# Kernel tuning notes

Measured on AMD Instinct MI355X. Metric: run time of the kernel, lower is better.

## Reference

```python
import jax, jax.numpy as jnp
import numpy as np

N = 4096   # node_each_graph == in_feats (adjacency-row node features)
H = 512    # n_hidden
C = 2      # n_classes
E = 65536  # edges (avg degree 16)
NL = 5     # n_layers -> 4 GINConv layers
NR = NL - 2  # stacked hidden GIN layers (layers 1..3)


def _bn(x, g, b, m, v):
    # BatchNorm1d in eval mode (running stats), eps=1e-5
    return (x - m) * jax.lax.rsqrt(v + 1e-5) * g + b


def setup_inputs():
    key = jax.random.key(0)
    ks = iter(jax.random.split(key, 16))
    nk = lambda: next(ks)
    s = 0.02
    f32 = jnp.float32
    d = {}
    d["feat"] = jax.random.normal(nk(), (N, N), f32)
    d["edge_src"] = jax.random.randint(nk(), (E,), 0, N)
    d["edge_dst"] = jax.random.randint(nk(), (E,), 0, N)
    # GIN layer 0: MLP is Linear(N,H)-BN-ReLU-Linear(H,H); ApplyNodeFunc BN; outer BN
    d["eps0"] = jnp.zeros((), f32)
    d["W0a"] = jax.random.normal(nk(), (N, H), f32) * s
    d["b0a"] = jnp.zeros((H,), f32)
    d["W0b"] = jax.random.normal(nk(), (H, H), f32) * s
    d["b0b"] = jnp.zeros((H,), f32)
    for nm in ["bn0a", "bnA0", "bnO0"]:
        d[nm + "_g"] = jnp.ones((H,), f32); d[nm + "_b"] = jnp.zeros((H,), f32)
        d[nm + "_m"] = jnp.zeros((H,), f32); d[nm + "_v"] = jnp.ones((H,), f32)
    # GIN layers 1..NL-2 stacked (H -> H)
    d["epsR"] = jnp.zeros((NR,), f32)
    d["WRa"] = jax.random.normal(nk(), (NR, H, H), f32) * s
    d["bRa"] = jnp.zeros((NR, H), f32)
    d["WRb"] = jax.random.normal(nk(), (NR, H, H), f32) * s
    d["bRb"] = jnp.zeros((NR, H), f32)
    for nm in ["bnRa", "bnAR", "bnOR"]:
        d[nm + "_g"] = jnp.ones((NR, H), f32); d[nm + "_b"] = jnp.zeros((NR, H), f32)
        d[nm + "_m"] = jnp.zeros((NR, H), f32); d[nm + "_v"] = jnp.ones((NR, H), f32)
    # per-hidden-rep readout linears (batch_size = 1)
    d["Wp0"] = jax.random.normal(nk(), (N * N, C), f32) * 0.001
    d["bp0"] = jnp.zeros((C,), f32)
    d["WpR"] = jax.random.normal(nk(), (NL - 1, N * H, C), f32) * 0.001
    d["bpR"] = jnp.zeros((NL - 1, C), f32)
    return d


def _gin(h, src, dst, eps, Wa, ba, bna, Wb, bb, bnA, bnO):
    # GINConv sum-aggregation: (1+eps)*h + sum over in-neighbors
    agg = jax.ops.segment_sum(h[src], dst, num_segments=N)
    x = (1.0 + eps) * h + agg
    # MLP (num_layers=2): Linear -> BN -> ReLU -> Linear
    x = jax.nn.relu(_bn(x @ Wa + ba, *bna))
    x = x @ Wb + bb
    # ApplyNodeFunc: BN -> ReLU
    x = jax.nn.relu(_bn(x, *bnA))
    # Model-level BN -> ReLU
    x = jax.nn.relu(_bn(x, *bnO))
    return x


def reference(feat, edge_src, edge_dst, eps0, W0a, b0a, W0b, b0b,
              bn0a_g, bn0a_b, bn0a_m, bn0a_v, bnA0_g, bnA0_b, bnA0_m, bnA0_v,
              bnO0_g, bnO0_b, bnO0_m, bnO0_v,
              epsR, WRa, bRa, WRb, bRb,
              bnRa_g, bnRa_b, bnRa_m, bnRa_v, bnAR_g, bnAR_b, bnAR_m, bnAR_v,
              bnOR_g, bnOR_b, bnOR_m, bnOR_v, Wp0, bp0, WpR, bpR):
    h = _gin(feat, edge_src, edge_dst, eps0, W0a, b0a,
             (bn0a_g, bn0a_b, bn0a_m, bn0a_v), W0b, b0b,
             (bnA0_g, bnA0_b, bnA0_m, bnA0_v), (bnO0_g, bnO0_b, bnO0_m, bnO0_v))
    hs = [h]
    for i in range(NR):  # small fixed layer loop
        h = _gin(h, edge_src, edge_dst, epsR[i], WRa[i], bRa[i],
                 (bnRa_g[i], bnRa_b[i], bnRa_m[i], bnRa_v[i]), WRb[i], bRb[i],
                 (bnAR_g[i], bnAR_b[i], bnAR_m[i], bnAR_v[i]),
                 (bnOR_g[i], bnOR_b[i], bnOR_m[i], bnOR_v[i]))
        hs.append(h)
    # jumping-knowledge readout over hidden_rep (eval: dropout = identity)
    score = feat.reshape(1, -1) @ Wp0 + bp0
    for i, hi in enumerate(hs):
        score = score + hi.reshape(1, -1) @ WpR[i] + bpR[i]
    return score
```

## Files before the change

kernel.cpp:

```cpp
#include <hip/hip_runtime.h>
#include <cstdint>
#include <cstddef>

typedef __attribute__((ext_vector_type(8))) short short8;
typedef __attribute__((ext_vector_type(4))) float f32x4;
typedef __attribute__((ext_vector_type(4))) float f4;
typedef __attribute__((ext_vector_type(2))) float f2;
typedef __attribute__((ext_vector_type(4))) unsigned short us4;

#define NN 4096
#define HH 512
#define EE 65536

#define GLOAD(gp, lp) __builtin_amdgcn_global_load_lds( \
    (const __attribute__((address_space(1))) void*)(gp), \
    (__attribute__((address_space(3))) void*)(lp), 16, 0, 0)

__device__ __forceinline__ unsigned short f2bf(float x) {
    union { float f; unsigned u; } un; un.f = x;
    unsigned r = un.u + 0x7fffu + ((un.u >> 16) & 1u);
    return (unsigned short)(r >> 16);
}
__device__ __forceinline__ float b2f(unsigned short v) {
    union { unsigned u; float f; } un; un.u = ((unsigned)v) << 16; return un.f;
}

__global__ __launch_bounds__(256) void k_prep(const float* __restrict__ feat,
                                              const float* __restrict__ Wp0,
                                              unsigned short* __restrict__ featb,
                                              float* __restrict__ part,
                                              const float* __restrict__ W0a,
                                              const float* __restrict__ W0b,
                                              const float* __restrict__ WRa,
                                              const float* __restrict__ WRb,
                                              unsigned short* __restrict__ w0at,
                                              unsigned short* __restrict__ wt,
                                              const int* __restrict__ edst,
                                              int* __restrict__ starts,
                                              int* __restrict__ cursor) {
    __shared__ alignas(16) f4 fs[1024];
    __shared__ float s0[256], s1[256];
    __shared__ int wtot4[4], woff4[4];
    const int t = threadIdx.x;
    const int bid = blockIdx.x;
    if (bid == 0) {
        int* cnt = (int*)fs;
        for (int i = t; i < NN; i += 256) { cnt[i] = 0; cursor[i] = 0; }
        __syncthreads();
        const int4* e4 = (const int4*)edst;
        for (int b = 0; b < 64; b += 8) {
            int4 v[8];
#pragma unroll
            for (int k = 0; k < 8; ++k)
                v[k] = e4[(b + k) * 256 + t];
#pragma unroll
            for (int k = 0; k < 8; ++k) {
                atomicAdd(&cnt[v[k].x], 1); atomicAdd(&cnt[v[k].y], 1);
                atomicAdd(&cnt[v[k].z], 1); atomicAdd(&cnt[v[k].w], 1);
            }
        }
        __syncthreads();
        const int base = t * 16;
        int c[16]; int s = 0;
#pragma unroll
        for (int i = 0; i < 16; ++i) { c[i] = cnt[base + i]; s += c[i]; }
        const int lane = t & 63, wv = t >> 6;
        int inc = s;
        for (int d = 1; d < 64; d <<= 1) {
            int v = __shfl_up(inc, d);
            if (lane >= d) inc += v;
        }
        if (lane == 63) wtot4[wv] = inc;
        __syncthreads();
        if (t == 0) {
            int a = 0;
            for (int i = 0; i < 4; ++i) { woff4[i] = a; a += wtot4[i]; }
            starts[NN] = a;
        }
        __syncthreads();
        int run = woff4[wv] + inc - s;
#pragma unroll
        for (int i = 0; i < 16; ++i) { starts[base + i] = run; run += c[i]; }
    } else if (bid <= 4096) {
        const int b2 = bid - 1;
        const long B0 = (long)b2 * 1024;
        const f4* ff = (const f4*)feat;
        const f4* ww = (const f4*)Wp0;
        f4 v[4];
#pragma unroll
        for (int k = 0; k < 4; ++k)
            v[k] = __builtin_nontemporal_load(ff + B0 + k * 256 + t);
#pragma unroll
        for (int k = 0; k < 4; ++k) {
            fs[k * 256 + t] = v[k];
            us4 o;
            o.x = f2bf(v[k].x); o.y = f2bf(v[k].y); o.z = f2bf(v[k].z); o.w = f2bf(v[k].w);
            __builtin_nontemporal_store(o, (us4*)featb + B0 + k * 256 + t);
        }
        f4 wv[8];
#pragma unroll
        for (int k = 0; k < 8; ++k)
            wv[k] = __builtin_nontemporal_load(ww + 2 * B0 + k * 256 + t);
        __syncthreads();
        float a0 = 0.f, a1 = 0.f;
#pragma unroll
        for (int k = 0; k < 8; ++k) {
            const int q = k * 256 + t;
            f2 fp = *(const f2*)((const char*)fs + (size_t)q * 8);
            a0 += fp.x * wv[k].x + fp.y * wv[k].z;
            a1 += fp.x * wv[k].y + fp.y * wv[k].w;
        }
        s0[t] = a0; s1[t] = a1;
        __syncthreads();
        for (int s = 128; s > 0; s >>= 1) {
            if (t < s) { s0[t] += s0[t + s]; s1[t] += s1[t + s]; }
            __syncthreads();
        }
        if (t == 0) { part[2 * b2] = s0[0]; part[2 * b2 + 1] = s1[0]; }
    } else {
        float (*tile)[33] = (float(*)[33])fs;
        const int tix = bid - 4097;
        const float* W; unsigned short* Wt; int K, kb, nb;
        if (tix < 2048) {
            W = W0a; Wt = w0at; K = NN; kb = tix >> 4; nb = tix & 15;
        } else {
            const int t2 = tix - 2048;
            const int z = t2 >> 8, r = t2 & 255;
            W = (z == 0) ? W0b : (z < 4) ? WRa + (size_t)(z - 1) * HH * HH
                                         : WRb + (size_t)(z - 4) * HH * HH;
            Wt = wt + (size_t)z * HH * HH; K = HH; kb = r >> 4; nb = r & 15;
        }
        const int k0 = kb * 32, n0 = nb * 32;
        const int tx = t & 31, ty = t >> 5;
        for (int r = ty; r < 32; r += 8)
            tile[r][tx] = W[(size_t)(k0 + r) * HH + n0 + tx];
        __syncthreads();
        for (int r = ty; r < 32; r += 8)
            Wt[(size_t)(n0 + r) * K + k0 + tx] = f2bf(tile[tx][r]);
    }
}

__global__ __launch_bounds__(256) void k_gemm0s(
    const unsigned short* __restrict__ A, const unsigned short* __restrict__ Bt,
    float* __restrict__ outf,
    const int* __restrict__ esrc, const int* __restrict__ edst,
    const int* __restrict__ starts, int* __restrict__ cursor, int* __restrict__ sorted)
{
    constexpr int K = NN, N = HH;
    __shared__ alignas(16) unsigned short As[2 * 8192];
    __shared__ alignas(16) unsigned short Bs[2 * 8192];
    const int bid = blockIdx.x;
    const int t = threadIdx.x;
    if (bid >= 512) {
        const int e = (bid - 512) * 256 + t;
        const int d = edst[e];
        const int p = starts[d] + atomicAdd(&cursor[d], 1);
        sorted[p] = esrc[e];
        return;
    }
    const int bx = bid & 31, by = (bid >> 5) & 3, bz = bid >> 7;
    const int lane = t & 63, w = t >> 6;
    const int wr = w >> 1, wc = w & 1;
    const int l15 = lane & 15, l4 = lane >> 4;
    const int m0 = bx * 128, n0 = by * 128;
    const int kbase = bz * (K / 4);

    f32x4 acc[4][4];
#pragma unroll
    for (int i = 0; i < 4; ++i)
#pragma unroll
        for (int j = 0; j < 4; ++j) acc[i][j] = (f32x4){0.f, 0.f, 0.f, 0.f};

    const int ar = t >> 3;
    const int ac = (t & 7) ^ (ar & 7);
    const unsigned short* ga = A + (size_t)(m0 + ar) * K + kbase + ac * 8;
    const unsigned short* gb = Bt + (size_t)(n0 + ar) * K + kbase + ac * 8;

    auto stage = [&](int kt, int buf) {
        const int ko = kt * 64;
        unsigned short* Ad = As + buf * 8192 + t * 8;
        unsigned short* Bd = Bs + buf * 8192 + t * 8;
        GLOAD(ga + ko, Ad);
        GLOAD(ga + (size_t)32 * K + ko, Ad + 2048);
        GLOAD(ga + (size_t)64 * K + ko, Ad + 4096);
        GLOAD(ga + (size_t)96 * K + ko, Ad + 6144);
        GLOAD(gb + ko, Bd);
        GLOAD(gb + (size_t)32 * K + ko, Bd + 2048);
        GLOAD(gb + (size_t)64 * K + ko, Bd + 4096);
        GLOAD(gb + (size_t)96 * K + ko, Bd + 6144);
    };

    const int rsw = l15 & 7;
    const int nk = (K / 4) >> 6;
    stage(0, 0);
    __syncthreads();
    for (int kt = 0; kt < nk; ++kt) {
        const int cur = kt & 1;
        if (kt + 1 < nk) stage(kt + 1, cur ^ 1);
        const unsigned short* Ac = As + cur * 8192;
        const unsigned short* Bc = Bs + cur * 8192;
        short8 aF[4][2], bF[4][2];
#pragma unroll
        for (int i = 0; i < 4; ++i)
#pragma unroll
            for (int ks = 0; ks < 2; ++ks)
                aF[i][ks] = *(const short8*)(Ac + (wr * 64 + i * 16 + l15) * 64
                                                + (((ks * 4 + l4) ^ rsw) * 8));
#pragma unroll
        for (int j = 0; j < 4; ++j)
#pragma unroll
            for (int ks = 0; ks < 2; ++ks)
                bF[j][ks] = *(const short8*)(Bc + (wc * 64 + j * 16 + l15) * 64
                                                + (((ks * 4 + l4) ^ rsw) * 8));
#pragma unroll
        for (int ks = 0; ks < 2; ++ks)
#pragma unroll
            for (int i = 0; i < 4; ++i)
#pragma unroll
                for (int j = 0; j < 4; ++j)
                    acc[i][j] = __builtin_amdgcn_mfma_f32_16x16x32_bf16(aF[i][ks], bF[j][ks], acc[i][j], 0, 0, 0);
        __syncthreads();
    }

    float* op = outf + (size_t)bz * NN * N;
    const int mrow = m0 + wr * 64;
#pragma unroll
    for (int j = 0; j < 4; ++j) {
        const int cg = n0 + wc * 64 + j * 16 + l15;
#pragma unroll
        for (int i = 0; i < 4; ++i)
#pragma unroll
            for (int r = 0; r < 4; ++r)
                op[(size_t)(mrow + i * 16 + l4 * 4 + r) * N + cg] = acc[i][j][r];
    }
}

#define SORTCAP 6144
__global__ __launch_bounds__(256) void k_redsortb(const float* __restrict__ p,
                                                  unsigned short* __restrict__ G0b,
                                                  const int* __restrict__ starts,
                                                  int* __restrict__ a) {
    __shared__ int buf[SORTCAP];
    const int bid = blockIdx.x;
    const int t = threadIdx.x;
    if (bid >= 2048) {
        const int binbase = (bid - 2048) * 256;
        const int lo = starts[binbase], hi = starts[binbase + 256];
        const int n = hi - lo;
        if (n <= SORTCAP) {
            for (int i = t; i < n; i += 256) buf[i] = a[lo + i];
            __syncthreads();
            const int d = binbase + t;
            const int s = starts[d] - lo, e = starts[d + 1] - lo;
            for (int i = s + 1; i < e; ++i) {
                int v = buf[i]; int j = i - 1;
                while (j >= s && buf[j] > v) { buf[j + 1] = buf[j]; --j; }
                buf[j + 1] = v;
            }
            __syncthreads();
            for (int i = t; i < n; i += 256) a[lo + i] = buf[i];
        } else {
            const int d = binbase + t;
            const int s = starts[d], e = starts[d + 1];
            for (int i = s + 1; i < e; ++i) {
                int v = a[i]; int j = i - 1;
                while (j >= s && a[j] > v) { a[j + 1] = a[j]; --j; }
                a[j + 1] = v;
            }
        }
        return;
    }
    const long S = (long)NN * HH / 4;
    long i = bid * 256L + t;
    float4 x = ((const float4*)p)[i];
    float4 y = ((const float4*)p)[i + S];
    float4 c = ((const float4*)p)[i + 2 * S];
    float4 d4 = ((const float4*)p)[i + 3 * S];
    us4 o;
    o.x = f2bf((x.x + y.x) + (c.x + d4.x));
    o.y = f2bf((x.y + y.y) + (c.y + d4.y));
    o.z = f2bf((x.z + y.z) + (c.z + d4.z));
    o.w = f2bf((x.w + y.w) + (c.w + d4.w));
    ((us4*)G0b)[i] = o;
}

template<int EPI, bool DOT>
__global__ __launch_bounds__(256) void k_gemmH(
    const unsigned short* __restrict__ A, const unsigned short* __restrict__ Bt,
    const float* __restrict__ bias,
    const float* __restrict__ g1, const float* __restrict__ b1,
    const float* __restrict__ m1, const float* __restrict__ v1,
    const float* __restrict__ g2, const float* __restrict__ b2,
    const float* __restrict__ m2, const float* __restrict__ v2,
    unsigned short* __restrict__ outb,
    const float* __restrict__ wq, float* __restrict__ part, int slotbase)
{
    constexpr int K = HH, N = HH;
    __shared__ alignas(16) unsigned short As[2 * 8192];
    __shared__ alignas(16) unsigned short Bs[2 * 4096];
    const int t = threadIdx.x;
    const int lane = t & 63, w = t >> 6;
    const int wr = w >> 1, wc = w & 1;
    const int l15 = lane & 15, l4 = lane >> 4;
    const int m0 = blockIdx.x * 128, n0 = blockIdx.y * 64;

    f32x4 acc[4][2];
#pragma unroll
    for (int i = 0; i < 4; ++i)
#pragma unroll
        for (int j = 0; j < 2; ++j) acc[i][j] = (f32x4){0.f, 0.f, 0.f, 0.f};

    const int ar = t >> 3;
    const int ac = (t & 7) ^ (ar & 7);
    const unsigned short* ga = A + (size_t)(m0 + ar) * K + ac * 8;
    const unsigned short* gb = Bt + (size_t)(n0 + ar) * K + ac * 8;

    auto stage = [&](int kt, int buf) {
        const int ko = kt * 64;
        unsigned short* Ad = As + buf * 8192 + t * 8;
        unsigned short* Bd = Bs + buf * 4096 + t * 8;
        GLOAD(ga + ko, Ad);
        GLOAD(ga + (size_t)32 * K + ko, Ad + 2048);
        GLOAD(ga + (size_t)64 * K + ko, Ad + 4096);
        GLOAD(ga + (size_t)96 * K + ko, Ad + 6144);
        GLOAD(gb + ko, Bd);
        GLOAD(gb + (size_t)32 * K + ko, Bd + 2048);
    };

    const int rsw = l15 & 7;
    const int nk = K >> 6;
    stage(0, 0);
    __syncthreads();
    for (int kt = 0; kt < nk; ++kt) {
        const int cur = kt & 1;
        if (kt + 1 < nk) stage(kt + 1, cur ^ 1);
        const unsigned short* Ac = As + cur * 8192;
        const unsigned short* Bc = Bs + cur * 4096;
        short8 aF[4][2], bF[2][2];
#pragma unroll
        for (int i = 0; i < 4; ++i)
#pragma unroll
            for (int ks = 0; ks < 2; ++ks)
                aF[i][ks] = *(const short8*)(Ac + (wr * 64 + i * 16 + l15) * 64
                                                + (((ks * 4 + l4) ^ rsw) * 8));
#pragma unroll
        for (int j = 0; j < 2; ++j)
#pragma unroll
            for (int ks = 0; ks < 2; ++ks)
                bF[j][ks] = *(const short8*)(Bc + (wc * 32 + j * 16 + l15) * 64
                                                + (((ks * 4 + l4) ^ rsw) * 8));
#pragma unroll
        for (int ks = 0; ks < 2; ++ks)
#pragma unroll
            for (int i = 0; i < 4; ++i)
#pragma unroll
                for (int j = 0; j < 2; ++j)
                    acc[i][j] = __builtin_amdgcn_mfma_f32_16x16x32_bf16(aF[i][ks], bF[j][ks], acc[i][j], 0, 0, 0);
        __syncthreads();
    }

    const int mrow = m0 + wr * 64;
    float d0 = 0.f, d1 = 0.f;
#pragma unroll
    for (int j = 0; j < 2; ++j) {
        const int cg = n0 + wc * 32 + j * 16 + l15;
        const float bi = bias[cg];
        const float sc1 = rsqrtf(v1[cg] + 1e-5f) * g1[cg];
        const float sh1 = b1[cg] - m1[cg] * sc1;
        float sc2 = 1.f, sh2 = 0.f;
        if (EPI == 3) {
            sc2 = rsqrtf(v2[cg] + 1e-5f) * g2[cg];
            sh2 = b2[cg] - m2[cg] * sc2;
        }
#pragma unroll
        for (int i = 0; i < 4; ++i) {
#pragma unroll
            for (int r = 0; r < 4; ++r) {
                const int rg = mrow + i * 16 + l4 * 4 + r;
                float x = acc[i][j][r];
                x = fmaxf((x + bi) * sc1 + sh1, 0.f);
                if (EPI == 3) x = fmaxf(x * sc2 + sh2, 0.f);
                outb[(size_t)rg * N + cg] = f2bf(x);
                if constexpr (DOT) {
                    f2 wvv = __builtin_nontemporal_load((const f2*)wq + (size_t)rg * N + cg);
                    d0 += x * wvv.x; d1 += x * wvv.y;
                }
            }
        }
    }
    if constexpr (DOT) {
        float* r0 = (float*)As;
        float* r1 = r0 + 256;
        __syncthreads();
        r0[t] = d0; r1[t] = d1;
        __syncthreads();
        for (int s = 128; s > 0; s >>= 1) {
            if (t < s) { r0[t] += r0[t + s]; r1[t] += r1[t + s]; }
            __syncthreads();
        }
        if (t == 0) {
            const int slot = slotbase + blockIdx.y * gridDim.x + blockIdx.x;
            part[2 * slot] = r0[0]; part[2 * slot + 1] = r1[0];
        }
    }
}

__global__ __launch_bounds__(128) void k_agg0(
    const unsigned short* __restrict__ G0, const int* __restrict__ starts,
    const int* __restrict__ sorted, const float* __restrict__ epsp,
    const float* __restrict__ bias,
    const float* __restrict__ bg, const float* __restrict__ bb,
    const float* __restrict__ bm, const float* __restrict__ bv,
    unsigned short* __restrict__ outb)
{
    const int d = blockIdx.x, t = threadIdx.x;
    const float ep = 1.0f + epsp[0];
    ushort4 ow = ((const ushort4*)(G0 + (size_t)d * HH))[t];
    float sx = 0.f, sy = 0.f, sz = 0.f, sw = 0.f;
    const int e0 = starts[d], e1 = starts[d + 1];
    int i = e0;
    for (; i + 4 <= e1; i += 4) {
        int q0 = sorted[i], q1 = sorted[i + 1], q2 = sorted[i + 2], q3 = sorted[i + 3];
        ushort4 x0 = ((const ushort4*)(G0 + (size_t)q0 * HH))[t];
        ushort4 x1 = ((const ushort4*)(G0 + (size_t)q1 * HH))[t];
        ushort4 x2 = ((const ushort4*)(G0 + (size_t)q2 * HH))[t];
        ushort4 x3 = ((const ushort4*)(G0 + (size_t)q3 * HH))[t];
        sx += (b2f(x0.x) + b2f(x1.x)) + (b2f(x2.x) + b2f(x3.x));
        sy += (b2f(x0.y) + b2f(x1.y)) + (b2f(x2.y) + b2f(x3.y));
        sz += (b2f(x0.z) + b2f(x1.z)) + (b2f(x2.z) + b2f(x3.z));
        sw += (b2f(x0.w) + b2f(x1.w)) + (b2f(x2.w) + b2f(x3.w));
    }
    for (; i < e1; ++i) {
        ushort4 x = ((const ushort4*)(G0 + (size_t)sorted[i] * HH))[t];
        sx += b2f(x.x); sy += b2f(x.y); sz += b2f(x.z); sw += b2f(x.w);
    }
    float4 bi = ((const float4*)bias)[t];
    float4 g4 = ((const float4*)bg)[t];
    float4 b4 = ((const float4*)bb)[t];
    float4 m4 = ((const float4*)bm)[t];
    float4 v4 = ((const float4*)bv)[t];
    float x0 = ep * b2f(ow.x) + sx + bi.x;
    float x1 = ep * b2f(ow.y) + sy + bi.y;
    float x2 = ep * b2f(ow.z) + sz + bi.z;
    float x3 = ep * b2f(ow.w) + sw + bi.w;
    x0 = fmaxf((x0 - m4.x) * rsqrtf(v4.x + 1e-5f) * g4.x + b4.x, 0.f);
    x1 = fmaxf((x1 - m4.y) * rsqrtf(v4.y + 1e-5f) * g4.y + b4.y, 0.f);
    x2 = fmaxf((x2 - m4.z) * rsqrtf(v4.z + 1e-5f) * g4.z + b4.z, 0.f);
    x3 = fmaxf((x3 - m4.w) * rsqrtf(v4.w + 1e-5f) * g4.w + b4.w, 0.f);
    ushort4 o; o.x = f2bf(x0); o.y = f2bf(x1); o.z = f2bf(x2); o.w = f2bf(x3);
    ((ushort4*)(outb + (size_t)d * HH))[t] = o;
}

__global__ __launch_bounds__(128) void k_aggL(
    const unsigned short* __restrict__ hsrc, const int* __restrict__ starts,
    const int* __restrict__ sorted, const float* __restrict__ epsp,
    unsigned short* __restrict__ outb)
{
    const int d = blockIdx.x, t = threadIdx.x;
    const float ep = 1.0f + epsp[0];
    ushort4 ow = ((const ushort4*)(hsrc + (size_t)d * HH))[t];
    float sx = 0.f, sy = 0.f, sz = 0.f, sw = 0.f;
    const int e0 = starts[d], e1 = starts[d + 1];
    int i = e0;
    for (; i + 4 <= e1; i += 4) {
        int q0 = sorted[i], q1 = sorted[i + 1], q2 = sorted[i + 2], q3 = sorted[i + 3];
        ushort4 x0 = ((const ushort4*)(hsrc + (size_t)q0 * HH))[t];
        ushort4 x1 = ((const ushort4*)(hsrc + (size_t)q1 * HH))[t];
        ushort4 x2 = ((const ushort4*)(hsrc + (size_t)q2 * HH))[t];
        ushort4 x3 = ((const ushort4*)(hsrc + (size_t)q3 * HH))[t];
        sx += (b2f(x0.x) + b2f(x1.x)) + (b2f(x2.x) + b2f(x3.x));
        sy += (b2f(x0.y) + b2f(x1.y)) + (b2f(x2.y) + b2f(x3.y));
        sz += (b2f(x0.z) + b2f(x1.z)) + (b2f(x2.z) + b2f(x3.z));
        sw += (b2f(x0.w) + b2f(x1.w)) + (b2f(x2.w) + b2f(x3.w));
    }
    for (; i < e1; ++i) {
        ushort4 x = ((const ushort4*)(hsrc + (size_t)sorted[i] * HH))[t];
        sx += b2f(x.x); sy += b2f(x.y); sz += b2f(x.z); sw += b2f(x.w);
    }
    ushort4 o;
    o.x = f2bf(ep * b2f(ow.x) + sx);
    o.y = f2bf(ep * b2f(ow.y) + sy);
    o.z = f2bf(ep * b2f(ow.z) + sz);
    o.w = f2bf(ep * b2f(ow.w) + sw);
    ((ushort4*)(outb + (size_t)d * HH))[t] = o;
}

__global__ __launch_bounds__(256) void k_final(const float* __restrict__ part, int nslot,
                                               const float* __restrict__ bp0, const float* __restrict__ bpR,
                                               float* __restrict__ out) {
    __shared__ float s0[256], s1[256];
    int t = threadIdx.x;
    float a0 = 0.f, a1 = 0.f;
    for (int i = t; i < nslot; i += 256) { a0 += part[2 * i]; a1 += part[2 * i + 1]; }
    s0[t] = a0; s1[t] = a1;
    __syncthreads();
    for (int s = 128; s > 0; s >>= 1) {
        if (t < s) { s0[t] += s0[t + s]; s1[t] += s1[t + s]; }
        __syncthreads();
    }
    if (t == 0) {
        out[0] = s0[0] + bp0[0] + bpR[0] + bpR[2] + bpR[4] + bpR[6];
        out[1] = s1[0] + bp0[1] + bpR[1] + bpR[3] + bpR[5] + bpR[7];
    }
}

extern "C" void kernel_launch(void* const* d_in, const int* in_sizes, int n_in,
                              void* d_out, int out_size, void* d_ws, size_t ws_size,
                              hipStream_t stream)
{
    const float* feat = (const float*)d_in[0];
    const int*   esrc = (const int*)d_in[1];
    const int*   edst = (const int*)d_in[2];
    const float* eps0 = (const float*)d_in[3];
    const float* W0a  = (const float*)d_in[4];
    const float* b0a  = (const float*)d_in[5];
    const float* W0b  = (const float*)d_in[6];
    const float* b0b  = (const float*)d_in[7];
    const float* bn0a_g = (const float*)d_in[8];
    const float* bn0a_b = (const float*)d_in[9];
    const float* bn0a_m = (const float*)d_in[10];
    const float* bn0a_v = (const float*)d_in[11];
    const float* bnA0_g = (const float*)d_in[12];
    const float* bnA0_b = (const float*)d_in[13];
    const float* bnA0_m = (const float*)d_in[14];
    const float* bnA0_v = (const float*)d_in[15];
    const float* bnO0_g = (const float*)d_in[16];
    const float* bnO0_b = (const float*)d_in[17];
    const float* bnO0_m = (const float*)d_in[18];
    const float* bnO0_v = (const float*)d_in[19];
    const float* epsR = (const float*)d_in[20];
    const float* WRa  = (const float*)d_in[21];
    const float* bRa  = (const float*)d_in[22];
    const float* WRb  = (const float*)d_in[23];
    const float* bRb  = (const float*)d_in[24];
    const float* bnRa_g = (const float*)d_in[25];
    const float* bnRa_b = (const float*)d_in[26];
    const float* bnRa_m = (const float*)d_in[27];
    const float* bnRa_v = (const float*)d_in[28];
    const float* bnAR_g = (const float*)d_in[29];
    const float* bnAR_b = (const float*)d_in[30];
    const float* bnAR_m = (const float*)d_in[31];
    const float* bnAR_v = (const float*)d_in[32];
    const float* bnOR_g = (const float*)d_in[33];
    const float* bnOR_b = (const float*)d_in[34];
    const float* bnOR_m = (const float*)d_in[35];
    const float* bnOR_v = (const float*)d_in[36];
    const float* Wp0 = (const float*)d_in[37];
    const float* bp0 = (const float*)d_in[38];
    const float* WpR = (const float*)d_in[39];
    const float* bpR = (const float*)d_in[40];
    float* out = (float*)d_out;

    char* ws = (char*)d_ws;
    const size_t MB = 1024 * 1024;
    int*   starts = (int*)(ws + 0x10000);
    int*   cursor = (int*)(ws + 0x20000);
    int*   sorted = (int*)(ws + 0x30000);
    float* part   = (float*)(ws + 0x70000);
    unsigned short* featb = (unsigned short*)(ws + 1 * MB);
    unsigned short* w0at  = (unsigned short*)(ws + 33 * MB);
    unsigned short* wt    = (unsigned short*)(ws + 37 * MB);
    unsigned short* G0b   = (unsigned short*)(ws + 41 * MB);
    unsigned short* xb = (unsigned short*)(ws + 49 * MB);
    unsigned short* yb = (unsigned short*)(ws + 53 * MB);
    unsigned short* hb = (unsigned short*)(ws + 57 * MB);
    float* pbuf = (float*)(ws + 57 * MB);

    k_prep<<<1 + 4096 + 3840, 256, 0, stream>>>(feat, Wp0, featb, part,
                                                W0a, W0b, WRa, WRb, w0at, wt,
                                                edst, starts, cursor);

    k_gemm0s<<<768, 256, 0, stream>>>(featb, w0at, pbuf, esrc, edst, starts, cursor, sorted);

    k_redsortb<<<2064, 256, 0, stream>>>(pbuf, G0b, starts, sorted);

    k_agg0<<<NN, 128, 0, stream>>>(G0b, starts, sorted, eps0, b0a,
                                   bn0a_g, bn0a_b, bn0a_m, bn0a_v, xb);

    const dim3 hg(32, 8);
    k_gemmH<3, true><<<hg, 256, 0, stream>>>(xb, wt,
        b0b, bnA0_g, bnA0_b, bnA0_m, bnA0_v, bnO0_g, bnO0_b, bnO0_m, bnO0_v,
        hb, WpR, part, 4096);

    for (int i = 0; i < 3; ++i) {
        const unsigned short* hp = hb + (size_t)i * NN * HH;
        unsigned short* hn = hb + (size_t)(i + 1) * NN * HH;
        k_aggL<<<NN, 128, 0, stream>>>(hp, starts, sorted, epsR + i, xb);
        k_gemmH<1, false><<<hg, 256, 0, stream>>>(xb, wt + (size_t)(1 + i) * HH * HH,
            bRa + (size_t)i * HH,
            bnRa_g + (size_t)i * HH, bnRa_b + (size_t)i * HH, bnRa_m + (size_t)i * HH, bnRa_v + (size_t)i * HH,
            nullptr, nullptr, nullptr, nullptr,
            yb, nullptr, nullptr, 0);
        k_gemmH<3, true><<<hg, 256, 0, stream>>>(yb, wt + (size_t)(4 + i) * HH * HH,
            bRb + (size_t)i * HH,
            bnAR_g + (size_t)i * HH, bnAR_b + (size_t)i * HH, bnAR_m + (size_t)i * HH, bnAR_v + (size_t)i * HH,
            bnOR_g + (size_t)i * HH, bnOR_b + (size_t)i * HH, bnOR_m + (size_t)i * HH, bnOR_v + (size_t)i * HH,
            hn, WpR + (size_t)(i + 1) * NN * HH * 2, part, 4096 + (i + 1) * 256);
    }

    k_final<<<1, 256, 0, stream>>>(part, 4096 + 4 * 256, bp0, bpR, out);
}
```

Before: 242.9 us.

## Skip dead last-layer store, add nontemporal hints, deepen gather unroll

Several small memory-side tweaks are applied together. The last hidden layer's bf16 output is no longer written, since only its readout dot product is consumed. GEMM0 partial outputs are stored, and their reduction loads are read, with nontemporal hints. The Wp0 loads in k_prep are hoisted before the conversion stores to expose more memory parallelism. Both neighbor-aggregation kernels now gather 8 rows per iteration instead of 4, which raises register use in exchange for more loads in flight.

```diff
diff --git a/kernel.cpp b/kernel.cpp
--- a/kernel.cpp
+++ b/kernel.cpp
@@ -86,10 +86,13 @@
         const long B0 = (long)b2 * 1024;
         const f4* ff = (const f4*)feat;
         const f4* ww = (const f4*)Wp0;
-        f4 v[4];
+        f4 v[4], wv[8];
 #pragma unroll
         for (int k = 0; k < 4; ++k)
             v[k] = __builtin_nontemporal_load(ff + B0 + k * 256 + t);
+#pragma unroll
+        for (int k = 0; k < 8; ++k)
+            wv[k] = __builtin_nontemporal_load(ww + 2 * B0 + k * 256 + t);
 #pragma unroll
         for (int k = 0; k < 4; ++k) {
             fs[k * 256 + t] = v[k];
@@ -97,10 +100,6 @@
             o.x = f2bf(v[k].x); o.y = f2bf(v[k].y); o.z = f2bf(v[k].z); o.w = f2bf(v[k].w);
             __builtin_nontemporal_store(o, (us4*)featb + B0 + k * 256 + t);
         }
-        f4 wv[8];
-#pragma unroll
-        for (int k = 0; k < 8; ++k)
-            wv[k] = __builtin_nontemporal_load(ww + 2 * B0 + k * 256 + t);
         __syncthreads();
         float a0 = 0.f, a1 = 0.f;
 #pragma unroll
@@ -231,7 +230,8 @@
         for (int i = 0; i < 4; ++i)
 #pragma unroll
             for (int r = 0; r < 4; ++r)
-                op[(size_t)(mrow + i * 16 + l4 * 4 + r) * N + cg] = acc[i][j][r];
+                __builtin_nontemporal_store(acc[i][j][r],
+                    op + (size_t)(mrow + i * 16 + l4 * 4 + r) * N + cg);
     }
 }
 
@@ -272,10 +272,11 @@
     }
     const long S = (long)NN * HH / 4;
     long i = bid * 256L + t;
-    float4 x = ((const float4*)p)[i];
-    float4 y = ((const float4*)p)[i + S];
-    float4 c = ((const float4*)p)[i + 2 * S];
-    float4 d4 = ((const float4*)p)[i + 3 * S];
+    const f4* pp = (const f4*)p;
+    f4 x = __builtin_nontemporal_load(pp + i);
+    f4 y = __builtin_nontemporal_load(pp + i + S);
+    f4 c = __builtin_nontemporal_load(pp + i + 2 * S);
+    f4 d4 = __builtin_nontemporal_load(pp + i + 3 * S);
     us4 o;
     o.x = f2bf((x.x + y.x) + (c.x + d4.x));
     o.y = f2bf((x.y + y.y) + (c.y + d4.y));
@@ -284,7 +285,7 @@
     ((us4*)G0b)[i] = o;
 }
 
-template<int EPI, bool DOT>
+template<int EPI, bool DOT, bool STOREH>
 __global__ __launch_bounds__(256) void k_gemmH(
     const unsigned short* __restrict__ A, const unsigned short* __restrict__ Bt,
     const float* __restrict__ bias,
@@ -380,7 +381,7 @@
                 float x = acc[i][j][r];
                 x = fmaxf((x + bi) * sc1 + sh1, 0.f);
                 if (EPI == 3) x = fmaxf(x * sc2 + sh2, 0.f);
-                outb[(size_t)rg * N + cg] = f2bf(x);
+                if constexpr (STOREH) outb[(size_t)rg * N + cg] = f2bf(x);
                 if constexpr (DOT) {
                     f2 wvv = __builtin_nontemporal_load((const f2*)wq + (size_t)rg * N + cg);
                     d0 += x * wvv.x; d1 += x * wvv.y;
@@ -419,16 +420,15 @@
     float sx = 0.f, sy = 0.f, sz = 0.f, sw = 0.f;
     const int e0 = starts[d], e1 = starts[d + 1];
     int i = e0;
-    for (; i + 4 <= e1; i += 4) {
-        int q0 = sorted[i], q1 = sorted[i + 1], q2 = sorted[i + 2], q3 = sorted[i + 3];
-        ushort4 x0 = ((const ushort4*)(G0 + (size_t)q0 * HH))[t];
-        ushort4 x1 = ((const ushort4*)(G0 + (size_t)q1 * HH))[t];
-        ushort4 x2 = ((const ushort4*)(G0 + (size_t)q2 * HH))[t];
-        ushort4 x3 = ((const ushort4*)(G0 + (size_t)q3 * HH))[t];
-        sx += (b2f(x0.x) + b2f(x1.x)) + (b2f(x2.x) + b2f(x3.x));
-        sy += (b2f(x0.y) + b2f(x1.y)) + (b2f(x2.y) + b2f(x3.y));
-        sz += (b2f(x0.z) + b2f(x1.z)) + (b2f(x2.z) + b2f(x3.z));
-        sw += (b2f(x0.w) + b2f(x1.w)) + (b2f(x2.w) + b2f(x3.w));
+    for (; i + 8 <= e1; i += 8) {
+        ushort4 x[8];
+#pragma unroll
+        for (int k = 0; k < 8; ++k)
+            x[k] = ((const ushort4*)(G0 + (size_t)sorted[i + k] * HH))[t];
+#pragma unroll
+        for (int k = 0; k < 8; ++k) {
+            sx += b2f(x[k].x); sy += b2f(x[k].y); sz += b2f(x[k].z); sw += b2f(x[k].w);
+        }
     }
     for (; i < e1; ++i) {
         ushort4 x = ((const ushort4*)(G0 + (size_t)sorted[i] * HH))[t];
@@ -462,16 +462,15 @@
     float sx = 0.f, sy = 0.f, sz = 0.f, sw = 0.f;
     const int e0 = starts[d], e1 = starts[d + 1];
     int i = e0;
-    for (; i + 4 <= e1; i += 4) {
-        int q0 = sorted[i], q1 = sorted[i + 1], q2 = sorted[i + 2], q3 = sorted[i + 3];
-        ushort4 x0 = ((const ushort4*)(hsrc + (size_t)q0 * HH))[t];
-        ushort4 x1 = ((const ushort4*)(hsrc + (size_t)q1 * HH))[t];
-        ushort4 x2 = ((const ushort4*)(hsrc + (size_t)q2 * HH))[t];
-        ushort4 x3 = ((const ushort4*)(hsrc + (size_t)q3 * HH))[t];
-        sx += (b2f(x0.x) + b2f(x1.x)) + (b2f(x2.x) + b2f(x3.x));
-        sy += (b2f(x0.y) + b2f(x1.y)) + (b2f(x2.y) + b2f(x3.y));
-        sz += (b2f(x0.z) + b2f(x1.z)) + (b2f(x2.z) + b2f(x3.z));
-        sw += (b2f(x0.w) + b2f(x1.w)) + (b2f(x2.w) + b2f(x3.w));
+    for (; i + 8 <= e1; i += 8) {
+        ushort4 x[8];
+#pragma unroll
+        for (int k = 0; k < 8; ++k)
+            x[k] = ((const ushort4*)(hsrc + (size_t)sorted[i + k] * HH))[t];
+#pragma unroll
+        for (int k = 0; k < 8; ++k) {
+            sx += b2f(x[k].x); sy += b2f(x[k].y); sz += b2f(x[k].z); sw += b2f(x[k].w);
+        }
     }
     for (; i < e1; ++i) {
         ushort4 x = ((const ushort4*)(hsrc + (size_t)sorted[i] * HH))[t];
@@ -578,7 +577,7 @@
                                    bn0a_g, bn0a_b, bn0a_m, bn0a_v, xb);
 
     const dim3 hg(32, 8);
-    k_gemmH<3, true><<<hg, 256, 0, stream>>>(xb, wt,
+    k_gemmH<3, true, true><<<hg, 256, 0, stream>>>(xb, wt,
         b0b, bnA0_g, bnA0_b, bnA0_m, bnA0_v, bnO0_g, bnO0_b, bnO0_m, bnO0_v,
         hb, WpR, part, 4096);
 
@@ -586,16 +585,24 @@
         const unsigned short* hp = hb + (size_t)i * NN * HH;
         unsigned short* hn = hb + (size_t)(i + 1) * NN * HH;
         k_aggL<<<NN, 128, 0, stream>>>(hp, starts, sorted, epsR + i, xb);
-        k_gemmH<1, false><<<hg, 256, 0, stream>>>(xb, wt + (size_t)(1 + i) * HH * HH,
+        k_gemmH<1, false, true><<<hg, 256, 0, stream>>>(xb, wt + (size_t)(1 + i) * HH * HH,
             bRa + (size_t)i * HH,
             bnRa_g + (size_t)i * HH, bnRa_b + (size_t)i * HH, bnRa_m + (size_t)i * HH, bnRa_v + (size_t)i * HH,
             nullptr, nullptr, nullptr, nullptr,
             yb, nullptr, nullptr, 0);
-        k_gemmH<3, true><<<hg, 256, 0, stream>>>(yb, wt + (size_t)(4 + i) * HH * HH,
-            bRb + (size_t)i * HH,
-            bnAR_g + (size_t)i * HH, bnAR_b + (size_t)i * HH, bnAR_m + (size_t)i * HH, bnAR_v + (size_t)i * HH,
-            bnOR_g + (size_t)i * HH, bnOR_b + (size_t)i * HH, bnOR_m + (size_t)i * HH, bnOR_v + (size_t)i * HH,
-            hn, WpR + (size_t)(i + 1) * NN * HH * 2, part, 4096 + (i + 1) * 256);
+        if (i < 2) {
+            k_gemmH<3, true, true><<<hg, 256, 0, stream>>>(yb, wt + (size_t)(4 + i) * HH * HH,
+                bRb + (size_t)i * HH,
+                bnAR_g + (size_t)i * HH, bnAR_b + (size_t)i * HH, bnAR_m + (size_t)i * HH, bnAR_v + (size_t)i * HH,
+                bnOR_g + (size_t)i * HH, bnOR_b + (size_t)i * HH, bnOR_m + (size_t)i * HH, bnOR_v + (size_t)i * HH,
+                hn, WpR + (size_t)(i + 1) * NN * HH * 2, part, 4096 + (i + 1) * 256);
+        } else {
+            k_gemmH<3, true, false><<<hg, 256, 0, stream>>>(yb, wt + (size_t)(4 + i) * HH * HH,
+                bRb + (size_t)i * HH,
+                bnAR_g + (size_t)i * HH, bnAR_b + (size_t)i * HH, bnAR_m + (size_t)i * HH, bnAR_v + (size_t)i * HH,
+                bnOR_g + (size_t)i * HH, bnOR_b + (size_t)i * HH, bnOR_m + (size_t)i * HH, bnOR_v + (size_t)i * HH,
+                nullptr, WpR + (size_t)(i + 1) * NN * HH * 2, part, 4096 + (i + 1) * 256);
+        }
     }
 
     k_final<<<1, 256, 0, stream>>>(part, 4096 + 4 * 256, bp0, bpR, out);
```

Result: no change. 243.0 us (+0.0%).
